# Performance work log

Measured on AMD Instinct MI355X. Metric: run time of the kernel, lower is better.

The kernel has to match this reference:

```python
import jax, jax.numpy as jnp
import numpy as np

DIM = 512
NUM_HEADS = 8
DIM_HEAD = DIM // NUM_HEADS


def _xavier(key, shape):
    fan_in, fan_out = shape[0], shape[1]
    a = (6.0 / (fan_in + fan_out)) ** 0.5
    return jax.random.uniform(key, shape, jnp.float32, -a, a)


def setup_inputs() -> dict:
    key = jax.random.key(0)
    ks = jax.random.split(key, 8)
    B, N, M = 2, 2048, 2048
    x = jax.random.normal(ks[0], (B, N, DIM), jnp.float32)
    source = jax.random.normal(ks[1], (B, M, DIM), jnp.float32)
    source_mask = jax.random.randint(ks[2], (B, M), 0, 2) > 0
    Wq = _xavier(ks[3], (DIM, DIM)); bq = jnp.zeros((DIM,), jnp.float32)
    Wk = _xavier(ks[4], (DIM, DIM)); bk = jnp.zeros((DIM,), jnp.float32)
    Wv = _xavier(ks[5], (DIM, DIM)); bv = jnp.zeros((DIM,), jnp.float32)
    Wm = _xavier(ks[6], (DIM, DIM)); bm = jnp.zeros((DIM,), jnp.float32)
    return {"x": x, "source": source, "source_mask": source_mask,
            "Wq": Wq, "bq": bq, "Wk": Wk, "bk": bk,
            "Wv": Wv, "bv": bv, "Wm": Wm, "bm": bm}


def reference(x, source, source_mask, Wq, bq, Wk, bk, Wv, bv, Wm, bm):
    B, N, D = x.shape
    M = source.shape[-2]
    H, Dh = NUM_HEADS, DIM_HEAD
    # projections (torch Linear: x @ W^T + b)
    q = (x @ Wq.T + bq).reshape(B, N, H, Dh)
    k = (source @ Wk.T + bk).reshape(B, M, H, Dh)
    v = (source @ Wv.T + bv).reshape(B, M, H, Dh)
    scale = 1.0 / (Dh ** 0.5)
    # scores: [B, N, M, H]
    scores = jnp.einsum('bnhd,bmhd->bnmh', q, k) * scale
    scores = jnp.where(source_mask[:, None, :, None], scores, -jnp.inf)
    prob = jax.nn.softmax(scores, axis=-2)  # softmax over m
    agg = jnp.einsum('bnmh,bmhd->bnhd', prob, v).reshape(B, N, D)
    return agg @ Wm.T + bm
```

## Files before the change

### kernel.cpp

```cpp
#include <hip/hip_runtime.h>
#include <hip/hip_bf16.h>

#define DIMF 512
#define NHEAD 8
#define DHEAD 64
#define BATCH 2
#define SEQN 2048
#define SEQM 2048
#define PKS 72
#define PPS 36

typedef unsigned short u16;
typedef __attribute__((ext_vector_type(8))) short bf16x8;
typedef __attribute__((ext_vector_type(4))) float f32x4;

static __device__ __forceinline__ u16 f2bf(float f) {
    unsigned u = __float_as_uint(f);
    u += 0x7FFF + ((u >> 16) & 1);
    return (u16)(u >> 16);
}
static __device__ __forceinline__ u16 f2bf_fast(float f) {
    return (u16)((__float_as_uint(f) + 0x8000u) >> 16);
}

static __device__ __forceinline__
void load16(const u16* g, u16* l) {
    __builtin_amdgcn_global_load_lds(
        (const __attribute__((address_space(1))) void*)g,
        (__attribute__((address_space(3))) void*)l,
        16, 0, 0);
}

__global__ __launch_bounds__(256)
void cvt_bf16(const float* __restrict__ x, const float* __restrict__ src,
              const float* __restrict__ wq, const float* __restrict__ wk,
              const float* __restrict__ wv, const float* __restrict__ wm,
              u16* __restrict__ xb, u16* __restrict__ srcb,
              u16* __restrict__ wqb, u16* __restrict__ wkb,
              u16* __restrict__ wvb, u16* __restrict__ wmb)
{
    const float* in; u16* out; int n;
    switch (blockIdx.y) {
        case 0: in = x;   out = xb;   n = BATCH * SEQN * DIMF; break;
        case 1: in = src; out = srcb; n = BATCH * SEQM * DIMF; break;
        case 2: in = wq;  out = wqb;  n = DIMF * DIMF; break;
        case 3: in = wk;  out = wkb;  n = DIMF * DIMF; break;
        case 4: in = wv;  out = wvb;  n = DIMF * DIMF; break;
        default:in = wm;  out = wmb;  n = DIMF * DIMF; break;
    }
    int i = (blockIdx.x * 256 + threadIdx.x) * 4;
    if (i >= n) return;
    float4 v = *(const float4*)&in[i];
    *(ushort4*)&out[i] = make_ushort4(f2bf(v.x), f2bf(v.y), f2bf(v.z), f2bf(v.w));
}

__device__ __forceinline__
void gemm_mfma(const u16* __restrict__ X, const u16* __restrict__ W,
               const float* __restrict__ bias, void* __restrict__ Out, int mode)
{
    __shared__ u16 As[64 * 32];
    __shared__ u16 Bs[128 * 32];

    const int tid  = threadIdx.x;
    const int wave = tid >> 6;
    const int lane = tid & 63;
    const int l15  = lane & 15;
    const int quad = lane >> 4;
    const int wm = wave & 1, wn = wave >> 1;
    const int r0 = blockIdx.x * 64, c0 = blockIdx.y * 128;

    const u16* Ab = X + (size_t)r0 * DIMF;
    const u16* Bb = W + (size_t)c0 * DIMF;

    f32x4 acc[2][4] = {};

    const int arow = tid >> 2, akc = (tid & 3) << 3;

    for (int k0 = 0; k0 < DIMF; k0 += 32) {
        __syncthreads();
        load16(Ab + arow * DIMF + k0 + akc, (u16*)((char*)As + wave * 1024));
        #pragma unroll
        for (int i = 0; i < 2; ++i) {
            int chunk = i * 256 + tid;
            int row = chunk >> 2, kc = (chunk & 3) << 3;
            load16(Bb + row * DIMF + k0 + kc,
                   (u16*)((char*)Bs + i * 4096 + wave * 1024));
        }
        __syncthreads();

        bf16x8 af[2], bf[4];
        #pragma unroll
        for (int mi = 0; mi < 2; ++mi)
            af[mi] = *(const bf16x8*)&As[(wm * 32 + mi * 16 + l15) * 32 + quad * 8];
        #pragma unroll
        for (int ni = 0; ni < 4; ++ni)
            bf[ni] = *(const bf16x8*)&Bs[(wn * 64 + ni * 16 + l15) * 32 + quad * 8];
        #pragma unroll
        for (int mi = 0; mi < 2; ++mi)
            #pragma unroll
            for (int ni = 0; ni < 4; ++ni)
                acc[mi][ni] = __builtin_amdgcn_mfma_f32_16x16x32_bf16(
                    af[mi], bf[ni], acc[mi][ni], 0, 0, 0);
    }

    float bb[4];
    #pragma unroll
    for (int ni = 0; ni < 4; ++ni)
        bb[ni] = bias[c0 + wn * 64 + ni * 16 + l15];

    #pragma unroll
    for (int mi = 0; mi < 2; ++mi) {
        const int Rbase = r0 + wm * 32 + mi * 16 + quad * 4;
        const int b = Rbase >> 11;
        const int nb = Rbase & (SEQN - 1);
        #pragma unroll
        for (int ni = 0; ni < 4; ++ni) {
            const int C = c0 + wn * 64 + ni * 16 + l15;
            const int h = C >> 6, d = C & 63;
            if (mode == 0) {
                u16* ow = (u16*)Out;
                #pragma unroll
                for (int r = 0; r < 4; ++r)
                    ow[(((size_t)(b * NHEAD + h) * SEQN) + nb + r) * DHEAD + d] =
                        f2bf((acc[mi][ni][r] + bb[ni]) * 0.125f);
            } else if (mode == 1) {
                u16* ow = (u16*)Out;
                #pragma unroll
                for (int r = 0; r < 4; ++r)
                    ow[(((size_t)(b * NHEAD + h) * SEQN) + nb + r) * DHEAD + d] =
                        f2bf(acc[mi][ni][r] + bb[ni]);
            } else if (mode == 2) {
                u16* ow = (u16*)Out;
                ushort4 w4 = make_ushort4(f2bf(acc[mi][ni][0] + bb[ni]),
                                          f2bf(acc[mi][ni][1] + bb[ni]),
                                          f2bf(acc[mi][ni][2] + bb[ni]),
                                          f2bf(acc[mi][ni][3] + bb[ni]));
                *(ushort4*)&ow[((size_t)(b * NHEAD + h) * DHEAD + d) * SEQM + nb] = w4;
            } else {
                float* ow = (float*)Out;
                #pragma unroll
                for (int r = 0; r < 4; ++r)
                    ow[(size_t)(Rbase + r) * DIMF + C] = acc[mi][ni][r] + bb[ni];
            }
        }
    }
}

__global__ __launch_bounds__(256, 4)
void qkv_proj(const u16* __restrict__ xb, const u16* __restrict__ srcb,
              const u16* __restrict__ wqb, const float* __restrict__ bq,
              const u16* __restrict__ wkb, const float* __restrict__ bk,
              const u16* __restrict__ wvb, const float* __restrict__ bv,
              u16* __restrict__ qw, u16* __restrict__ kw, u16* __restrict__ vtw)
{
    const int z = blockIdx.z;
    const u16* X = (z == 0) ? xb  : srcb;
    const u16* W = (z == 0) ? wqb : (z == 1) ? wkb : wvb;
    const float* B = (z == 0) ? bq : (z == 1) ? bk : bv;
    void* O = (z == 0) ? (void*)qw : (z == 1) ? (void*)kw : (void*)vtw;
    gemm_mfma(X, W, B, O, z);
}

__global__ __launch_bounds__(256, 4)
void out_proj(const u16* __restrict__ aggb, const u16* __restrict__ wmb,
              const float* __restrict__ bm, float* __restrict__ out)
{
    gemm_mfma(aggb, wmb, bm, (void*)out, 3);
}

__global__ __launch_bounds__(256, 5)
void flash_attn_mfma(const u16* __restrict__ q, const u16* __restrict__ k,
                     const u16* __restrict__ vt, const int* __restrict__ mask,
                     u16* __restrict__ agg)
{
    __shared__ u16 Ks[64 * PKS];
    __shared__ u16 Vts[64 * PKS];
    __shared__ __align__(16) char UN[8448];
    u16*   Ps   = (u16*)UN;
    float* Osum = (float*)UN;
    float* Lsum = (float*)(UN + 8192);

    const int tid  = threadIdx.x;
    const int wave = tid >> 6;
    const int lane = tid & 63;
    const int l15  = lane & 15;
    const int quad = lane >> 4;
    const int qg = wave >> 1, mh = wave & 1;
    const int qt = blockIdx.x, h = blockIdx.y, b = blockIdx.z;
    const int n0 = qt * 32;
    const size_t hoff = (size_t)(b * NHEAD + h) * (size_t)SEQM * DHEAD;
    const u16* kb = k  + hoff;
    const u16* vb = vt + hoff;
    const int* mg = mask + b * SEQM;

    const int sr0 = tid >> 3,        sc0 = (tid & 7) << 3;
    const int sr1 = 32 + (tid >> 3), sc1 = sc0;

    bf16x8 qf[2];
    {
        const u16* qp = q + hoff + (size_t)(n0 + qg * 16 + l15) * DHEAD + quad * 8;
        qf[0] = *(const bf16x8*)qp;
        qf[1] = *(const bf16x8*)(qp + 32);
    }

    bf16x8 kn0, kn1, vn0, vn1;
    int mn;
    kn0 = *(const bf16x8*)&kb[(size_t)sr0 * DHEAD + sc0];
    kn1 = *(const bf16x8*)&kb[(size_t)sr1 * DHEAD + sc1];
    vn0 = *(const bf16x8*)&vb[(size_t)sr0 * SEQM + sc0];
    vn1 = *(const bf16x8*)&vb[(size_t)sr1 * SEQM + sc1];
    mn  = mg[lane];

    f32x4 O[4] = {};
    float psum = 0.f;

    for (int mt = 0; mt < SEQM / 64; ++mt) {
        const int m0 = mt * 64;
        bf16x8 kc0 = kn0, kc1 = kn1, vc0 = vn0, vc1 = vn1;
        unsigned long long mbits = __ballot(mn != 0);
        if (mt + 1 < SEQM / 64) {
            const int m1 = m0 + 64;
            kn0 = *(const bf16x8*)&kb[(size_t)(m1 + sr0) * DHEAD + sc0];
            kn1 = *(const bf16x8*)&kb[(size_t)(m1 + sr1) * DHEAD + sc1];
            vn0 = *(const bf16x8*)&vb[(size_t)sr0 * SEQM + m1 + sc0];
            vn1 = *(const bf16x8*)&vb[(size_t)sr1 * SEQM + m1 + sc1];
            mn  = mg[m1 + lane];
        }
        __syncthreads();
        *(bf16x8*)&Ks[sr0 * PKS + sc0]  = kc0;
        *(bf16x8*)&Ks[sr1 * PKS + sc1]  = kc1;
        *(bf16x8*)&Vts[sr0 * PKS + sc0] = vc0;
        *(bf16x8*)&Vts[sr1 * PKS + sc1] = vc1;
        __syncthreads();

        f32x4 st[2] = {};
        #pragma unroll
        for (int sub = 0; sub < 2; ++sub) {
            #pragma unroll
            for (int c = 0; c < 2; ++c) {
                bf16x8 af = *(const bf16x8*)&Ks[(32 * mh + 16 * sub + l15) * PKS + 32 * c + quad * 8];
                st[sub] = __builtin_amdgcn_mfma_f32_16x16x32_bf16(af, qf[c], st[sub], 0, 0, 0);
            }
        }

        u16 pb[2][4];
        #pragma unroll
        for (int sub = 0; sub < 2; ++sub)
            #pragma unroll
            for (int r = 0; r < 4; ++r) {
                int bit = (int)((mbits >> (32 * mh + 16 * sub + 4 * quad + r)) & 1ULL);
                float sv = bit ? st[sub][r] : -1e30f;
                float p = __expf(sv);
                psum += p;
                pb[sub][r] = f2bf_fast(p);
            }

        u16* Pw = Ps + wave * (16 * PPS);
        #pragma unroll
        for (int sub = 0; sub < 2; ++sub) {
            ushort4 w4 = make_ushort4(pb[sub][0], pb[sub][1], pb[sub][2], pb[sub][3]);
            *(ushort4*)&Pw[l15 * PPS + 16 * sub + 4 * quad] = w4;
        }

        bf16x8 pf = *(const bf16x8*)&Pw[l15 * PPS + quad * 8];
        #pragma unroll
        for (int sd = 0; sd < 4; ++sd) {
            bf16x8 vf = *(const bf16x8*)&Vts[(16 * sd + l15) * PKS + 32 * mh + quad * 8];
            O[sd] = __builtin_amdgcn_mfma_f32_16x16x32_bf16(pf, vf, O[sd], 0, 0, 0);
        }
    }

    psum += __shfl_xor(psum, 16);
    psum += __shfl_xor(psum, 32);

    __syncthreads();
    if (mh == 1) {
        #pragma unroll
        for (int sd = 0; sd < 4; ++sd)
            #pragma unroll
            for (int r = 0; r < 4; ++r)
                Osum[qg * 1024 + (quad * 4 + r) * 64 + 16 * sd + l15] = O[sd][r];
        if (quad == 0) Lsum[qg * 16 + l15] = psum;
    }
    __syncthreads();
    if (mh == 0) {
        float l_tot = psum + Lsum[qg * 16 + l15];
        float lr4[4];
        #pragma unroll
        for (int r = 0; r < 4; ++r) lr4[r] = __shfl(l_tot, quad * 4 + r);
        #pragma unroll
        for (int r = 0; r < 4; ++r) {
            const int n = n0 + qg * 16 + quad * 4 + r;
            const float inv = 1.f / lr4[r];
            u16* ag = agg + ((size_t)b * SEQN + n) * DIMF + h * DHEAD + l15;
            #pragma unroll
            for (int sd = 0; sd < 4; ++sd)
                ag[16 * sd] = f2bf((O[sd][r] +
                                    Osum[qg * 1024 + (quad * 4 + r) * 64 + 16 * sd + l15]) * inv);
        }
    }
}

extern "C" void kernel_launch(void* const* d_in, const int* in_sizes, int n_in,
                              void* d_out, int out_size, void* d_ws, size_t ws_size,
                              hipStream_t stream)
{
    (void)in_sizes; (void)n_in; (void)out_size; (void)ws_size;
    const float* x      = (const float*)d_in[0];
    const float* source = (const float*)d_in[1];
    const int*   mask   = (const int*)  d_in[2];
    const float* Wq = (const float*)d_in[3]; const float* bq = (const float*)d_in[4];
    const float* Wk = (const float*)d_in[5]; const float* bk = (const float*)d_in[6];
    const float* Wv = (const float*)d_in[7]; const float* bv = (const float*)d_in[8];
    const float* Wm = (const float*)d_in[9]; const float* bm = (const float*)d_in[10];
    float* out = (float*)d_out;

    const size_t SZ = (size_t)BATCH * SEQN * DIMF;
    const size_t WZ = (size_t)DIMF * DIMF;
    u16* qw   = (u16*)d_ws;
    u16* kw   = qw  + SZ;
    u16* vtw  = kw  + SZ;
    u16* xb   = vtw + SZ;
    u16* aggb = xb;
    u16* srcb = xb  + SZ;
    u16* wqb  = srcb + SZ;
    u16* wkb  = wqb + WZ;
    u16* wvb  = wkb + WZ;
    u16* wmb  = wvb + WZ;

    dim3 gcvt((SZ / 4 + 255) / 256, 6);
    cvt_bf16<<<gcvt, 256, 0, stream>>>(x, source, Wq, Wk, Wv, Wm,
                                       xb, srcb, wqb, wkb, wvb, wmb);

    dim3 gproj(4096 / 64, 512 / 128, 3);
    qkv_proj<<<gproj, 256, 0, stream>>>(xb, srcb, wqb, bq, wkb, bk, wvb, bv,
                                        qw, kw, vtw);

    dim3 gattn(SEQN / 32, NHEAD, BATCH);
    flash_attn_mfma<<<gattn, 256, 0, stream>>>(qw, kw, vtw, mask, aggb);

    dim3 gout(4096 / 64, 512 / 128);
    out_proj<<<gout, 256, 0, stream>>>(aggb, wmb, bm, out);
}
```

Before: 164.5 us.

## Fold key mask into V and an MFMA row-sum, drop LDS staging in attention

Masking moves out of the softmax loop. V rows are zeroed by the mask in the projection epilogue, and the softmax denominator is computed as an MFMA of P against a bf16 mask vector, which removes the per-element ballot/select and the scalar psum. The attention kernel now gives each wave 16 queries over the full key range and reads K/V fragments straight from global memory instead of staging them through shared memory. The cross-wave reduction and block syncs are gone. V is transposed by a separate small kernel, which adds a launch and extra global traffic, and the direct global K/V loads give up LDS reuse across waves.

```diff
diff --git a/kernel.cpp b/kernel.cpp
--- a/kernel.cpp
+++ b/kernel.cpp
@@ -7,8 +7,7 @@
 #define BATCH 2
 #define SEQN 2048
 #define SEQM 2048
-#define PKS 72
-#define PPS 36
+#define PPS 72
 
 typedef unsigned short u16;
 typedef __attribute__((ext_vector_type(8))) short bf16x8;
@@ -35,10 +34,20 @@
 void cvt_bf16(const float* __restrict__ x, const float* __restrict__ src,
               const float* __restrict__ wq, const float* __restrict__ wk,
               const float* __restrict__ wv, const float* __restrict__ wm,
+              const int* __restrict__ mask,
               u16* __restrict__ xb, u16* __restrict__ srcb,
               u16* __restrict__ wqb, u16* __restrict__ wkb,
-              u16* __restrict__ wvb, u16* __restrict__ wmb)
-{
+              u16* __restrict__ wvb, u16* __restrict__ wmb,
+              u16* __restrict__ maskbf)
+{
+    int i = (blockIdx.x * 256 + threadIdx.x) * 4;
+    if (blockIdx.y == 6) {
+        if (i >= BATCH * SEQM) return;
+        int4 m4 = *(const int4*)&mask[i];
+        *(ushort4*)&maskbf[i] = make_ushort4(m4.x ? 0x3F80 : 0, m4.y ? 0x3F80 : 0,
+                                             m4.z ? 0x3F80 : 0, m4.w ? 0x3F80 : 0);
+        return;
+    }
     const float* in; u16* out; int n;
     switch (blockIdx.y) {
         case 0: in = x;   out = xb;   n = BATCH * SEQN * DIMF; break;
@@ -48,7 +57,6 @@
         case 4: in = wv;  out = wvb;  n = DIMF * DIMF; break;
         default:in = wm;  out = wmb;  n = DIMF * DIMF; break;
     }
-    int i = (blockIdx.x * 256 + threadIdx.x) * 4;
     if (i >= n) return;
     float4 v = *(const float4*)&in[i];
     *(ushort4*)&out[i] = make_ushort4(f2bf(v.x), f2bf(v.y), f2bf(v.z), f2bf(v.w));
@@ -56,7 +64,8 @@
 
 __device__ __forceinline__
 void gemm_mfma(const u16* __restrict__ X, const u16* __restrict__ W,
-               const float* __restrict__ bias, void* __restrict__ Out, int mode)
+               const float* __restrict__ bias, const int* __restrict__ msk,
+               void* __restrict__ Out, int mode)
 {
     __shared__ u16 As[64 * 32];
     __shared__ u16 Bs[128 * 32];
@@ -73,7 +82,6 @@
     const u16* Bb = W + (size_t)c0 * DIMF;
 
     f32x4 acc[2][4] = {};
-
     const int arow = tid >> 2, akc = (tid & 3) << 3;
 
     for (int k0 = 0; k0 < DIMF; k0 += 32) {
@@ -113,6 +121,12 @@
         const int Rbase = r0 + wm * 32 + mi * 16 + quad * 4;
         const int b = Rbase >> 11;
         const int nb = Rbase & (SEQN - 1);
+        float mm[4] = {1.f, 1.f, 1.f, 1.f};
+        if (mode == 2) {
+            int4 m4 = *(const int4*)&msk[b * SEQM + nb];
+            mm[0] = m4.x ? 1.f : 0.f; mm[1] = m4.y ? 1.f : 0.f;
+            mm[2] = m4.z ? 1.f : 0.f; mm[3] = m4.w ? 1.f : 0.f;
+        }
         #pragma unroll
         for (int ni = 0; ni < 4; ++ni) {
             const int C = c0 + wn * 64 + ni * 16 + l15;
@@ -131,11 +145,10 @@
                         f2bf(acc[mi][ni][r] + bb[ni]);
             } else if (mode == 2) {
                 u16* ow = (u16*)Out;
-                ushort4 w4 = make_ushort4(f2bf(acc[mi][ni][0] + bb[ni]),
-                                          f2bf(acc[mi][ni][1] + bb[ni]),
-                                          f2bf(acc[mi][ni][2] + bb[ni]),
-                                          f2bf(acc[mi][ni][3] + bb[ni]));
-                *(ushort4*)&ow[((size_t)(b * NHEAD + h) * DHEAD + d) * SEQM + nb] = w4;
+                #pragma unroll
+                for (int r = 0; r < 4; ++r)
+                    ow[(((size_t)(b * NHEAD + h) * SEQN) + nb + r) * DHEAD + d] =
+                        f2bf((acc[mi][ni][r] + bb[ni]) * mm[r]);
             } else {
                 float* ow = (float*)Out;
                 #pragma unroll
@@ -151,153 +164,118 @@
               const u16* __restrict__ wqb, const float* __restrict__ bq,
               const u16* __restrict__ wkb, const float* __restrict__ bk,
               const u16* __restrict__ wvb, const float* __restrict__ bv,
-              u16* __restrict__ qw, u16* __restrict__ kw, u16* __restrict__ vtw)
+              const int* __restrict__ mask,
+              u16* __restrict__ qw, u16* __restrict__ kw, u16* __restrict__ vw)
 {
     const int z = blockIdx.z;
     const u16* X = (z == 0) ? xb  : srcb;
     const u16* W = (z == 0) ? wqb : (z == 1) ? wkb : wvb;
     const float* B = (z == 0) ? bq : (z == 1) ? bk : bv;
-    void* O = (z == 0) ? (void*)qw : (z == 1) ? (void*)kw : (void*)vtw;
-    gemm_mfma(X, W, B, O, z);
+    void* O = (z == 0) ? (void*)qw : (z == 1) ? (void*)kw : (void*)vw;
+    gemm_mfma(X, W, B, mask, O, z);
 }
 
 __global__ __launch_bounds__(256, 4)
 void out_proj(const u16* __restrict__ aggb, const u16* __restrict__ wmb,
               const float* __restrict__ bm, float* __restrict__ out)
 {
-    gemm_mfma(aggb, wmb, bm, (void*)out, 3);
-}
-
-__global__ __launch_bounds__(256, 5)
+    gemm_mfma(aggb, wmb, bm, nullptr, (void*)out, 3);
+}
+
+__global__ __launch_bounds__(256)
+void vtr(const u16* __restrict__ v, u16* __restrict__ vt)
+{
+    __shared__ u16 T[64 * 72];
+    const int tid = threadIdx.x;
+    const int m0 = blockIdx.x * 64, bh = blockIdx.y;
+    const u16* src = v + ((size_t)bh * SEQM + m0) * DHEAD;
+    const int r = tid >> 3, c = (tid & 7) << 3;
+    *(bf16x8*)&T[r * 72 + c]        = *(const bf16x8*)&src[r * DHEAD + c];
+    *(bf16x8*)&T[(r + 32) * 72 + c] = *(const bf16x8*)&src[(r + 32) * DHEAD + c];
+    __syncthreads();
+    const int d = tid >> 2, mc = (tid & 3) << 4;
+    u16 tmp[16];
+    #pragma unroll
+    for (int j = 0; j < 16; ++j) tmp[j] = T[(mc + j) * 72 + d];
+    u16* dst = vt + ((size_t)bh * DHEAD + d) * SEQM + m0 + mc;
+    *(bf16x8*)&dst[0] = *(bf16x8*)&tmp[0];
+    *(bf16x8*)&dst[8] = *(bf16x8*)&tmp[8];
+}
+
+__global__ __launch_bounds__(256, 2)
 void flash_attn_mfma(const u16* __restrict__ q, const u16* __restrict__ k,
-                     const u16* __restrict__ vt, const int* __restrict__ mask,
+                     const u16* __restrict__ vt, const u16* __restrict__ maskbf,
                      u16* __restrict__ agg)
 {
-    __shared__ u16 Ks[64 * PKS];
-    __shared__ u16 Vts[64 * PKS];
-    __shared__ __align__(16) char UN[8448];
-    u16*   Ps   = (u16*)UN;
-    float* Osum = (float*)UN;
-    float* Lsum = (float*)(UN + 8192);
+    __shared__ u16 Ps[4][16 * PPS];
 
     const int tid  = threadIdx.x;
     const int wave = tid >> 6;
     const int lane = tid & 63;
     const int l15  = lane & 15;
     const int quad = lane >> 4;
-    const int qg = wave >> 1, mh = wave & 1;
-    const int qt = blockIdx.x, h = blockIdx.y, b = blockIdx.z;
-    const int n0 = qt * 32;
+    const int w  = blockIdx.x * 4 + wave;
+    const int qt = w & 127;
+    const int h  = (w >> 7) & 7;
+    const int b  = w >> 10;
+    const int n0 = qt * 16;
     const size_t hoff = (size_t)(b * NHEAD + h) * (size_t)SEQM * DHEAD;
     const u16* kb = k  + hoff;
     const u16* vb = vt + hoff;
-    const int* mg = mask + b * SEQM;
-
-    const int sr0 = tid >> 3,        sc0 = (tid & 7) << 3;
-    const int sr1 = 32 + (tid >> 3), sc1 = sc0;
+    const u16* mb = maskbf + b * SEQM;
+    u16* Pw = &Ps[wave][0];
 
     bf16x8 qf[2];
     {
-        const u16* qp = q + hoff + (size_t)(n0 + qg * 16 + l15) * DHEAD + quad * 8;
+        const u16* qp = q + hoff + (size_t)(n0 + l15) * DHEAD + quad * 8;
         qf[0] = *(const bf16x8*)qp;
         qf[1] = *(const bf16x8*)(qp + 32);
     }
 
-    bf16x8 kn0, kn1, vn0, vn1;
-    int mn;
-    kn0 = *(const bf16x8*)&kb[(size_t)sr0 * DHEAD + sc0];
-    kn1 = *(const bf16x8*)&kb[(size_t)sr1 * DHEAD + sc1];
-    vn0 = *(const bf16x8*)&vb[(size_t)sr0 * SEQM + sc0];
-    vn1 = *(const bf16x8*)&vb[(size_t)sr1 * SEQM + sc1];
-    mn  = mg[lane];
-
     f32x4 O[4] = {};
-    float psum = 0.f;
-
-    for (int mt = 0; mt < SEQM / 64; ++mt) {
-        const int m0 = mt * 64;
-        bf16x8 kc0 = kn0, kc1 = kn1, vc0 = vn0, vc1 = vn1;
-        unsigned long long mbits = __ballot(mn != 0);
-        if (mt + 1 < SEQM / 64) {
-            const int m1 = m0 + 64;
-            kn0 = *(const bf16x8*)&kb[(size_t)(m1 + sr0) * DHEAD + sc0];
-            kn1 = *(const bf16x8*)&kb[(size_t)(m1 + sr1) * DHEAD + sc1];
-            vn0 = *(const bf16x8*)&vb[(size_t)sr0 * SEQM + m1 + sc0];
-            vn1 = *(const bf16x8*)&vb[(size_t)sr1 * SEQM + m1 + sc1];
-            mn  = mg[m1 + lane];
-        }
-        __syncthreads();
-        *(bf16x8*)&Ks[sr0 * PKS + sc0]  = kc0;
-        *(bf16x8*)&Ks[sr1 * PKS + sc1]  = kc1;
-        *(bf16x8*)&Vts[sr0 * PKS + sc0] = vc0;
-        *(bf16x8*)&Vts[sr1 * PKS + sc1] = vc1;
-        __syncthreads();
-
-        f32x4 st[2] = {};
-        #pragma unroll
-        for (int sub = 0; sub < 2; ++sub) {
+    f32x4 lacc = {};
+
+    for (int m0 = 0; m0 < SEQM; m0 += 64) {
+        f32x4 st[4] = {};
+        #pragma unroll
+        for (int sub = 0; sub < 4; ++sub) {
             #pragma unroll
             for (int c = 0; c < 2; ++c) {
-                bf16x8 af = *(const bf16x8*)&Ks[(32 * mh + 16 * sub + l15) * PKS + 32 * c + quad * 8];
+                bf16x8 af = *(const bf16x8*)
+                    &kb[(size_t)(m0 + 16 * sub + l15) * DHEAD + 32 * c + quad * 8];
                 st[sub] = __builtin_amdgcn_mfma_f32_16x16x32_bf16(af, qf[c], st[sub], 0, 0, 0);
             }
         }
-
-        u16 pb[2][4];
-        #pragma unroll
-        for (int sub = 0; sub < 2; ++sub)
+        #pragma unroll
+        for (int sub = 0; sub < 4; ++sub) {
+            ushort4 w4 = make_ushort4(f2bf_fast(__expf(st[sub][0])),
+                                      f2bf_fast(__expf(st[sub][1])),
+                                      f2bf_fast(__expf(st[sub][2])),
+                                      f2bf_fast(__expf(st[sub][3])));
+            *(ushort4*)&Pw[l15 * PPS + 16 * sub + 4 * quad] = w4;
+        }
+        #pragma unroll
+        for (int kh = 0; kh < 2; ++kh) {
+            bf16x8 pf = *(const bf16x8*)&Pw[l15 * PPS + kh * 32 + quad * 8];
+            bf16x8 mf = *(const bf16x8*)&mb[m0 + kh * 32 + quad * 8];
+            lacc = __builtin_amdgcn_mfma_f32_16x16x32_bf16(pf, mf, lacc, 0, 0, 0);
             #pragma unroll
-            for (int r = 0; r < 4; ++r) {
-                int bit = (int)((mbits >> (32 * mh + 16 * sub + 4 * quad + r)) & 1ULL);
-                float sv = bit ? st[sub][r] : -1e30f;
-                float p = __expf(sv);
-                psum += p;
-                pb[sub][r] = f2bf_fast(p);
+            for (int sd = 0; sd < 4; ++sd) {
+                bf16x8 vf = *(const bf16x8*)
+                    &vb[(size_t)(16 * sd + l15) * SEQM + m0 + kh * 32 + quad * 8];
+                O[sd] = __builtin_amdgcn_mfma_f32_16x16x32_bf16(pf, vf, O[sd], 0, 0, 0);
             }
-
-        u16* Pw = Ps + wave * (16 * PPS);
-        #pragma unroll
-        for (int sub = 0; sub < 2; ++sub) {
-            ushort4 w4 = make_ushort4(pb[sub][0], pb[sub][1], pb[sub][2], pb[sub][3]);
-            *(ushort4*)&Pw[l15 * PPS + 16 * sub + 4 * quad] = w4;
-        }
-
-        bf16x8 pf = *(const bf16x8*)&Pw[l15 * PPS + quad * 8];
-        #pragma unroll
-        for (int sd = 0; sd < 4; ++sd) {
-            bf16x8 vf = *(const bf16x8*)&Vts[(16 * sd + l15) * PKS + 32 * mh + quad * 8];
-            O[sd] = __builtin_amdgcn_mfma_f32_16x16x32_bf16(pf, vf, O[sd], 0, 0, 0);
-        }
-    }
-
-    psum += __shfl_xor(psum, 16);
-    psum += __shfl_xor(psum, 32);
-
-    __syncthreads();
-    if (mh == 1) {
+        }
+    }
+
+    #pragma unroll
+    for (int r = 0; r < 4; ++r) {
+        const float inv = 1.f / lacc[r];
+        const int n = n0 + quad * 4 + r;
+        u16* ag = agg + ((size_t)b * SEQN + n) * DIMF + h * DHEAD + l15;
         #pragma unroll
         for (int sd = 0; sd < 4; ++sd)
-            #pragma unroll
-            for (int r = 0; r < 4; ++r)
-                Osum[qg * 1024 + (quad * 4 + r) * 64 + 16 * sd + l15] = O[sd][r];
-        if (quad == 0) Lsum[qg * 16 + l15] = psum;
-    }
-    __syncthreads();
-    if (mh == 0) {
-        float l_tot = psum + Lsum[qg * 16 + l15];
-        float lr4[4];
-        #pragma unroll
-        for (int r = 0; r < 4; ++r) lr4[r] = __shfl(l_tot, quad * 4 + r);
-        #pragma unroll
-        for (int r = 0; r < 4; ++r) {
-            const int n = n0 + qg * 16 + quad * 4 + r;
-            const float inv = 1.f / lr4[r];
-            u16* ag = agg + ((size_t)b * SEQN + n) * DIMF + h * DHEAD + l15;
-            #pragma unroll
-            for (int sd = 0; sd < 4; ++sd)
-                ag[16 * sd] = f2bf((O[sd][r] +
-                                    Osum[qg * 1024 + (quad * 4 + r) * 64 + 16 * sd + l15]) * inv);
-        }
+            ag[16 * sd] = f2bf(O[sd][r] * inv);
     }
 }
 
@@ -319,25 +297,30 @@
     const size_t WZ = (size_t)DIMF * DIMF;
     u16* qw   = (u16*)d_ws;
     u16* kw   = qw  + SZ;
-    u16* vtw  = kw  + SZ;
-    u16* xb   = vtw + SZ;
-    u16* aggb = xb;
+    u16* vw   = kw  + SZ;
+    u16* aggb = vw;
+    u16* xb   = vw  + SZ;
+    u16* vtw  = xb;
     u16* srcb = xb  + SZ;
     u16* wqb  = srcb + SZ;
     u16* wkb  = wqb + WZ;
     u16* wvb  = wkb + WZ;
     u16* wmb  = wvb + WZ;
-
-    dim3 gcvt((SZ / 4 + 255) / 256, 6);
-    cvt_bf16<<<gcvt, 256, 0, stream>>>(x, source, Wq, Wk, Wv, Wm,
-                                       xb, srcb, wqb, wkb, wvb, wmb);
+    u16* maskbf = wmb + WZ;
+
+    dim3 gcvt((SZ / 4 + 255) / 256, 7);
+    cvt_bf16<<<gcvt, 256, 0, stream>>>(x, source, Wq, Wk, Wv, Wm, mask,
+                                       xb, srcb, wqb, wkb, wvb, wmb, maskbf);
 
     dim3 gproj(4096 / 64, 512 / 128, 3);
     qkv_proj<<<gproj, 256, 0, stream>>>(xb, srcb, wqb, bq, wkb, bk, wvb, bv,
-                                        qw, kw, vtw);
-
-    dim3 gattn(SEQN / 32, NHEAD, BATCH);
-    flash_attn_mfma<<<gattn, 256, 0, stream>>>(qw, kw, vtw, mask, aggb);
+                                        mask, qw, kw, vw);
+
+    dim3 gvtr(SEQM / 64, BATCH * NHEAD);
+    vtr<<<gvtr, 256, 0, stream>>>(vw, vtw);
+
+    dim3 gattn(2048 / 4);
+    flash_attn_mfma<<<gattn, 256, 0, stream>>>(qw, kw, vtw, maskbf, aggb);
 
     dim3 gout(4096 / 64, 512 / 128);
     out_proj<<<gout, 256, 0, stream>>>(aggb, wmb, bm, out);
```

After: 236.6 us. 43.8% more time.
